# Kernel tuning notes

Hardware: AMD Instinct MI355X
Metric: run time of the kernel (lower is better)

## Reference

```python
import jax, jax.numpy as jnp
import numpy as np

N, E, D, R = 8192, 131072, 128, 32
SIZES = (3, 5, 7)  # per-degree component counts (2l+1)
LN_EPS = 1e-5


def setup_inputs() -> dict:
    key = jax.random.key(0)
    ks = jax.random.split(key, 20)
    rn = lambda k, shape, s=1.0: jax.random.normal(k, shape, jnp.float32) * s
    inp = {
        'X0': rn(ks[0], (N, SIZES[0], D)),
        'X1': rn(ks[1], (N, SIZES[1], D)),
        'X2': rn(ks[2], (N, SIZES[2], D)),
        't_ij': rn(ks[3], (E, D)),
        'r0': rn(ks[4], (E, SIZES[0])),
        'r1': rn(ks[5], (E, SIZES[1])),
        'r2': rn(ks[6], (E, SIZES[2])),
        'edge_index': jax.random.randint(ks[7], (2, E), 0, N, dtype=jnp.int32),
        # params
        'W_vq': rn(ks[8], (D, R), D ** -0.5),
        'W_vk0': rn(ks[9], (D, R), D ** -0.5),
        'W_vk1': rn(ks[10], (D, R), D ** -0.5),
        'W_vk2': rn(ks[11], (D, R), D ** -0.5),
        'ln_g': jnp.ones((R,), jnp.float32),
        'ln_b': jnp.zeros((R,), jnp.float32),
        'W_w': rn(ks[12], (R, D), R ** -0.5),
        'b_w': jnp.zeros((D,), jnp.float32),
        'W_t1': rn(ks[13], (D, D), D ** -0.5),
        'b_t1': jnp.zeros((D,), jnp.float32),
        'W_t2': rn(ks[14], (D, D), D ** -0.5),
        'b_t2': jnp.zeros((D,), jnp.float32),
    }
    return inp


def _vec_rej(x, r):
    # x: [E, L, R], r: [E, L]; dot over component dim (L), keepdim, subtract projection
    r = r[..., None]
    dot = jnp.sum(x * r, axis=1, keepdims=True)  # [E, 1, R]
    return x - dot * r


def reference(X0, X1, X2, t_ij, r0, r1, r2, edge_index,
              W_vq, W_vk0, W_vk1, W_vk2, ln_g, ln_b, W_w, b_w,
              W_t1, b_t1, W_t2, b_t2):
    n_j, n_i = edge_index[0], edge_index[1]
    X_ls = jnp.concatenate([X0, X1, X2], axis=1)                 # [N, 15, D]
    eq_i = jnp.einsum('nld,dr->nlr', X_ls, W_vq)[n_i]            # [E, 15, R]
    ek = jnp.concatenate([
        jnp.einsum('nld,dr->nlr', X0, W_vk0),
        jnp.einsum('nld,dr->nlr', X1, W_vk1),
        jnp.einsum('nld,dr->nlr', X2, W_vk2)], axis=1)
    ek_j = ek[n_j]                                               # [E, 15, R]
    # per-degree vector rejection (vec_rej=True)
    qs, ksl, off = [], [], 0
    for r in (r0, r1, r2):
        s = r.shape[1]
        qs.append(_vec_rej(eq_i[:, off:off + s], r))
        ksl.append(_vec_rej(ek_j[:, off:off + s], -r))
        off += s
    eq_i = jnp.concatenate(qs, axis=1)
    ek_j = jnp.concatenate(ksl, axis=1)
    w_ij = jnp.sum(eq_i * ek_j, axis=1)                          # [E, R]
    # mlp_w = LayerNorm + Linear
    mu = jnp.mean(w_ij, axis=-1, keepdims=True)
    var = jnp.var(w_ij, axis=-1, keepdims=True)
    wn = (w_ij - mu) * jax.lax.rsqrt(var + LN_EPS) * ln_g + ln_b
    dw = wn @ W_w + b_w                                          # [E, D]
    # mlp_t = Linear -> silu -> Linear, then outer activation
    t = jax.nn.silu(t_ij @ W_t1 + b_t1) @ W_t2 + b_t2            # [E, D]
    return dw * jax.nn.silu(t)
```

## Files before the change

kernel.cpp:

```cpp
#include <hip/hip_runtime.h>
#include <hip/hip_bf16.h>

#define N_NODES 8192
#define N_EDGES 131072
#define LN_EPS  1e-5f

typedef __attribute__((ext_vector_type(8))) short bf16x8;
typedef __attribute__((ext_vector_type(4))) short bf16x4;
typedef __attribute__((ext_vector_type(4))) float f32x4;

__device__ __forceinline__ float silu_f(float x) {
    return x * __builtin_amdgcn_rcpf(1.0f + __expf(-x));
}

__device__ __forceinline__ unsigned short f2bf(float x) {
    union { float f; unsigned int u; } v; v.f = x;
    unsigned int r = v.u + 0x7FFFu + ((v.u >> 16) & 1u);
    return (unsigned short)(r >> 16);
}
__device__ __forceinline__ float bf2f(unsigned short u) {
    union { float f; unsigned int x; } v; v.x = ((unsigned int)u) << 16;
    return v.f;
}
__device__ __forceinline__ unsigned int pk2(float a, float b) {
    float2 t; t.x = a; t.y = b;
    union { __hip_bfloat162 h; unsigned int u; } v;
    v.h = __float22bfloat162_rn(t);
    return v.u;
}
__device__ __forceinline__ bf16x8 pack8(float4 u, float4 v) {
    union { bf16x8 b; unsigned int w[4]; } o;
    o.w[0] = pk2(u.x, u.y); o.w[1] = pk2(u.z, u.w);
    o.w[2] = pk2(v.x, v.y); o.w[3] = pk2(v.z, v.w);
    return o.b;
}
__device__ __forceinline__ bf16x4 pack4(float a, float b, float c, float d) {
    union { bf16x4 v; unsigned int u[2]; } o;
    o.u[0] = pk2(a, b); o.u[1] = pk2(c, d);
    return o.v;
}
__device__ __forceinline__ f32x4 mfma16(bf16x8 a, bf16x8 b, f32x4 c) {
    return __builtin_amdgcn_mfma_f32_16x16x32_bf16(a, b, c, 0, 0, 0);
}
#if __has_builtin(__builtin_amdgcn_mfma_f32_16x16x16bf16_1k)
__device__ __forceinline__ f32x4 mfma_k16(bf16x4 a, bf16x4 b, f32x4 c) {
    return __builtin_amdgcn_mfma_f32_16x16x16bf16_1k(a, b, c, 0, 0, 0);
}
#else
__device__ __forceinline__ f32x4 mfma_k16(bf16x4 a, bf16x4 b, f32x4 c) {
    f32x4 d;
    asm("v_mfma_f32_16x16x16_bf16 %0, %1, %2, %3"
        : "=v"(d) : "v"(a), "v"(b), "v"(c));
    return d;
}
#endif

__global__ __launch_bounds__(256) void prep_kernel(
    const float* __restrict__ W_w, const float* __restrict__ W_t1,
    const float* __restrict__ W_t2, const float* __restrict__ Wvq,
    const float* __restrict__ Wvk0, const float* __restrict__ Wvk1,
    const float* __restrict__ Wvk2,
    unsigned short* __restrict__ Wtw, unsigned short* __restrict__ Wt1b,
    unsigned short* __restrict__ Wt2b, unsigned short* __restrict__ Wqt,
    unsigned short* __restrict__ Wk0t, unsigned short* __restrict__ Wk1t,
    unsigned short* __restrict__ Wk2t)
{
    int i = blockIdx.x * 256 + threadIdx.x;
    if (i < 16384) {
        int n = i >> 7, k = i & 127;
        Wt1b[i] = f2bf(W_t1[k * 128 + n]);
        Wt2b[i] = f2bf(W_t2[k * 128 + n]);
    }
    if (i < 4096) {
        { int n = i >> 5, k = i & 31; Wtw[i] = f2bf(W_w[k * 128 + n]); }
        int r = i >> 7, d = i & 127;
        Wqt[i]  = f2bf(Wvq [d * 32 + r]);
        Wk0t[i] = f2bf(Wvk0[d * 32 + r]);
        Wk1t[i] = f2bf(Wvk1[d * 32 + r]);
        Wk2t[i] = f2bf(Wvk2[d * 32 + r]);
    }
}

template<int S, int LOFF>
__device__ __forceinline__ void proj_body(
    const float* __restrict__ X, const unsigned short* __restrict__ Wqt,
    const unsigned short* __restrict__ Wkt,
    unsigned short* __restrict__ eq, unsigned short* __restrict__ ek,
    int row0)
{
    const int tid  = threadIdx.x;
    const int lane = tid & 63;
    const int wv   = tid >> 6;
    const int l15  = lane & 15;
    const int lk   = lane >> 4;
    const int xrow = row0 + wv * 16 + l15;

    bf16x8 xf[4];
    #pragma unroll
    for (int kt = 0; kt < 4; ++kt) {
        const float* p = X + (size_t)xrow * 128 + kt * 32 + lk * 8;
        xf[kt] = pack8(*(const float4*)p, *(const float4*)(p + 4));
    }

    f32x4 qa[2], ka[2];
    #pragma unroll
    for (int h = 0; h < 2; ++h) {
        qa[h] = (f32x4){0.f, 0.f, 0.f, 0.f};
        ka[h] = (f32x4){0.f, 0.f, 0.f, 0.f};
    }
    #pragma unroll
    for (int kt = 0; kt < 4; ++kt) {
        #pragma unroll
        for (int h = 0; h < 2; ++h) {
            bf16x8 wq = *(const bf16x8*)&Wqt[(h * 16 + l15) * 128 + kt * 32 + lk * 8];
            bf16x8 wk = *(const bf16x8*)&Wkt[(h * 16 + l15) * 128 + kt * 32 + lk * 8];
            qa[h] = mfma16(wq, xf[kt], qa[h]);
            ka[h] = mfma16(wk, xf[kt], ka[h]);
        }
    }

    const int n = xrow / S;
    const int l = xrow % S + LOFF;
    const size_t base = (size_t)n * 512 + (size_t)l * 32;
    #pragma unroll
    for (int h = 0; h < 2; ++h) {
        union { ushort4 s; unsigned int u[2]; } pq, pk_;
        pq.u[0]  = pk2(qa[h][0], qa[h][1]); pq.u[1]  = pk2(qa[h][2], qa[h][3]);
        pk_.u[0] = pk2(ka[h][0], ka[h][1]); pk_.u[1] = pk2(ka[h][2], ka[h][3]);
        *(ushort4*)&eq[base + h * 16 + lk * 4] = pq.s;
        *(ushort4*)&ek[base + h * 16 + lk * 4] = pk_.s;
    }
}

__global__ __launch_bounds__(256) void proj_kernel(
    const float* __restrict__ X0, const float* __restrict__ X1,
    const float* __restrict__ X2,
    const unsigned short* __restrict__ Wqt,
    const unsigned short* __restrict__ Wk0t,
    const unsigned short* __restrict__ Wk1t,
    const unsigned short* __restrict__ Wk2t,
    unsigned short* __restrict__ eq, unsigned short* __restrict__ ek)
{
    const int b = blockIdx.x;
    if (b < 384)
        proj_body<3, 0>(X0, Wqt, Wk0t, eq, ek, b * 64);
    else if (b < 1024)
        proj_body<5, 3>(X1, Wqt, Wk1t, eq, ek, (b - 384) * 64);
    else
        proj_body<7, 8>(X2, Wqt, Wk2t, eq, ek, (b - 1024) * 64);
}

__device__ __forceinline__ float edge_w_f(
    const float* qv, const float* kv, const float* rv)
{
    float qk = 0.f;
    #pragma unroll
    for (int l = 0; l < 15; ++l) qk = fmaf(qv[l], kv[l], qk);
    float c0 = 2.f, c1 = 2.f, c2 = 2.f;
    #pragma unroll
    for (int l = 0; l < 3; ++l)  c0 -= rv[l] * rv[l];
    #pragma unroll
    for (int l = 3; l < 8; ++l)  c1 -= rv[l] * rv[l];
    #pragma unroll
    for (int l = 8; l < 15; ++l) c2 -= rv[l] * rv[l];
    float dq0 = 0.f, dk0 = 0.f, dq1 = 0.f, dk1 = 0.f, dq2 = 0.f, dk2 = 0.f;
    #pragma unroll
    for (int l = 0; l < 3; ++l)  { dq0 = fmaf(qv[l], rv[l], dq0); dk0 = fmaf(kv[l], rv[l], dk0); }
    #pragma unroll
    for (int l = 3; l < 8; ++l)  { dq1 = fmaf(qv[l], rv[l], dq1); dk1 = fmaf(kv[l], rv[l], dk1); }
    #pragma unroll
    for (int l = 8; l < 15; ++l) { dq2 = fmaf(qv[l], rv[l], dq2); dk2 = fmaf(kv[l], rv[l], dk2); }
    return qk - dq0 * dk0 * c0 - dq1 * dk1 * c1 - dq2 * dk2 * c2;
}

__global__ __launch_bounds__(256) void wn_kernel(
    const unsigned short* __restrict__ eq, const unsigned short* __restrict__ ek,
    const float* __restrict__ r0, const float* __restrict__ r1,
    const float* __restrict__ r2, const int* __restrict__ eidx,
    const float* __restrict__ ln_g, const float* __restrict__ ln_b,
    unsigned short* __restrict__ wn)
{
    const int tid = threadIdx.x;
    const int r   = tid & 31;
    const int hw  = tid >> 5;
    const int e0  = blockIdx.x * 16 + hw * 2;
    const int e1  = e0 + 1;
    const float g  = ln_g[r];
    const float bb = ln_b[r];

    const int nj0 = eidx[e0], ni0 = eidx[N_EDGES + e0];
    const int nj1 = eidx[e1], ni1 = eidx[N_EDGES + e1];

    const unsigned short* qp0 = eq + (size_t)ni0 * 512 + r;
    const unsigned short* kp0 = ek + (size_t)nj0 * 512 + r;
    const unsigned short* qp1 = eq + (size_t)ni1 * 512 + r;
    const unsigned short* kp1 = ek + (size_t)nj1 * 512 + r;

    float qv0[15], kv0[15], qv1[15], kv1[15];
    #pragma unroll
    for (int l = 0; l < 15; ++l) {
        qv0[l] = bf2f(qp0[l * 32]);
        kv0[l] = bf2f(kp0[l * 32]);
        qv1[l] = bf2f(qp1[l * 32]);
        kv1[l] = bf2f(kp1[l * 32]);
    }

    float rva[15], rvb[15];
    #pragma unroll
    for (int c = 0; c < 3; ++c) { rva[c]     = r0[e0 * 3 + c]; rvb[c]     = r0[e1 * 3 + c]; }
    #pragma unroll
    for (int c = 0; c < 5; ++c) { rva[3 + c] = r1[e0 * 5 + c]; rvb[3 + c] = r1[e1 * 5 + c]; }
    #pragma unroll
    for (int c = 0; c < 7; ++c) { rva[8 + c] = r2[e0 * 7 + c]; rvb[8 + c] = r2[e1 * 7 + c]; }

    const float w0 = edge_w_f(qv0, kv0, rva);
    const float w1 = edge_w_f(qv1, kv1, rvb);

    float s0 = w0, s20 = w0 * w0, s1 = w1, s21 = w1 * w1;
    #pragma unroll
    for (int off = 1; off < 32; off <<= 1) {
        s0  += __shfl_xor(s0,  off); s20 += __shfl_xor(s20, off);
        s1  += __shfl_xor(s1,  off); s21 += __shfl_xor(s21, off);
    }
    const float mu0   = s0 * (1.f / 32.f);
    const float var0  = s20 * (1.f / 32.f) - mu0 * mu0;
    const float mu1   = s1 * (1.f / 32.f);
    const float var1  = s21 * (1.f / 32.f) - mu1 * mu1;
    wn[(size_t)e0 * 32 + r] = f2bf((w0 - mu0) * rsqrtf(var0 + LN_EPS) * g + bb);
    wn[(size_t)e1 * 32 + r] = f2bf((w1 - mu1) * rsqrtf(var1 + LN_EPS) * g + bb);
}

__global__ __launch_bounds__(512, 4) void edge_kernel(
    const float* __restrict__ t_ij,
    const unsigned short* __restrict__ wn,
    const unsigned short* __restrict__ Wtw, const float* __restrict__ b_w,
    const unsigned short* __restrict__ Wt1, const float* __restrict__ b_t1,
    const unsigned short* __restrict__ Wt2, const float* __restrict__ b_t2,
    float* __restrict__ out)
{
    __shared__ __align__(16) unsigned short W1l[16384];
    __shared__ __align__(16) unsigned short W2l[16384];
    __shared__ __align__(16) unsigned short Wwl[4096];

    const int tid  = threadIdx.x;
    const int lane = tid & 63;
    const int wv   = tid >> 6;
    const int l15  = lane & 15;
    const int lk   = lane >> 4;
    const int tile = (blockIdx.x * 8 + wv) * 32;
    const int swz7 = (l15 & 7) << 4;
    const int swz3 = (l15 & 3) << 4;

    #pragma unroll
    for (int i = 0; i < 4; ++i) {
        const int c   = tid + i * 512;
        const int row = c >> 4, c16 = c & 15;
        const int off = (row * 256 + c16 * 16) ^ ((row & 7) << 4);
        *(uint4*)((char*)W1l + off) = *(const uint4*)&Wt1[row * 128 + c16 * 8];
        *(uint4*)((char*)W2l + off) = *(const uint4*)&Wt2[row * 128 + c16 * 8];
    }
    {
        const int c   = tid;
        const int row = c >> 2, c4 = c & 3;
        uint4 v = *(const uint4*)&Wtw[row * 32 + c4 * 8];
        *(uint4*)((char*)Wwl + ((row * 64 + c4 * 16) ^ ((row & 3) << 4))) = v;
    }

    bf16x8 a1[4][2];
    #pragma unroll
    for (int kt = 0; kt < 4; ++kt)
        #pragma unroll
        for (int rt = 0; rt < 2; ++rt) {
            const float* p = t_ij + (size_t)(tile + rt * 16 + l15) * 128
                           + kt * 32 + lk * 8;
            a1[kt][rt] = pack8(*(const float4*)p, *(const float4*)(p + 4));
        }

    bf16x8 wnf[2];
    #pragma unroll
    for (int rt = 0; rt < 2; ++rt)
        wnf[rt] = *(const bf16x8*)&wn[(size_t)(tile + rt * 16 + l15) * 32 + lk * 8];

    __syncthreads();

    bf16x4 h[2][8];
    #pragma unroll
    for (int ct = 0; ct < 8; ++ct) {
        bf16x8 w1f[4];
        #pragma unroll
        for (int kt = 0; kt < 4; ++kt)
            w1f[kt] = *(const bf16x8*)((const char*)W1l +
                (((ct * 16 + l15) * 256 + kt * 64 + lk * 16) ^ swz7));
        f32x4 ac[2];
        #pragma unroll
        for (int rt = 0; rt < 2; ++rt) ac[rt] = (f32x4){0.f, 0.f, 0.f, 0.f};
        #pragma unroll
        for (int kt = 0; kt < 4; ++kt)
            #pragma unroll
            for (int rt = 0; rt < 2; ++rt)
                ac[rt] = mfma16(w1f[kt], a1[kt][rt], ac[rt]);

        const float4 bt1 = *(const float4*)&b_t1[ct * 16 + lk * 4];
        #pragma unroll
        for (int rt = 0; rt < 2; ++rt)
            h[rt][ct] = pack4(silu_f(ac[rt][0] + bt1.x),
                              silu_f(ac[rt][1] + bt1.y),
                              silu_f(ac[rt][2] + bt1.z),
                              silu_f(ac[rt][3] + bt1.w));
    }

    #pragma unroll
    for (int ct2 = 0; ct2 < 8; ++ct2) {
        bf16x4 w2b[8];
        #pragma unroll
        for (int ct1 = 0; ct1 < 8; ++ct1)
            w2b[ct1] = *(const bf16x4*)((const char*)W2l +
                (((ct2 * 16 + l15) * 256 + ct1 * 32 + lk * 8) ^ swz7));
        bf16x8 wwf = *(const bf16x8*)((const char*)Wwl +
            (((ct2 * 16 + l15) * 64 + lk * 16) ^ swz3));
        const float bwv = b_w[ct2 * 16 + l15];
        const float b2v = b_t2[ct2 * 16 + l15];

        #pragma unroll
        for (int rt = 0; rt < 2; ++rt) {
            f32x4 o = (f32x4){0.f, 0.f, 0.f, 0.f};
            #pragma unroll
            for (int ct1 = 0; ct1 < 8; ++ct1)
                o = mfma_k16(h[rt][ct1], w2b[ct1], o);
            f32x4 d = mfma16(wnf[rt], wwf, (f32x4){0.f, 0.f, 0.f, 0.f});

            float* op = out + (size_t)(tile + rt * 16 + lk * 4) * 128
                      + ct2 * 16 + l15;
            #pragma unroll
            for (int j = 0; j < 4; ++j)
                op[j * 128] = (d[j] + bwv) * silu_f(o[j] + b2v);
        }
    }
}

extern "C" void kernel_launch(void* const* d_in, const int* in_sizes, int n_in,
                              void* d_out, int out_size, void* d_ws, size_t ws_size,
                              hipStream_t stream) {
    (void)in_sizes; (void)n_in; (void)out_size; (void)ws_size;
    const float* X0   = (const float*)d_in[0];
    const float* X1   = (const float*)d_in[1];
    const float* X2   = (const float*)d_in[2];
    const float* t_ij = (const float*)d_in[3];
    const float* r0   = (const float*)d_in[4];
    const float* r1   = (const float*)d_in[5];
    const float* r2   = (const float*)d_in[6];
    const int*   eidx = (const int*)d_in[7];
    const float* Wvq  = (const float*)d_in[8];
    const float* Wvk0 = (const float*)d_in[9];
    const float* Wvk1 = (const float*)d_in[10];
    const float* Wvk2 = (const float*)d_in[11];
    const float* ln_g = (const float*)d_in[12];
    const float* ln_b = (const float*)d_in[13];
    const float* W_w  = (const float*)d_in[14];
    const float* b_w  = (const float*)d_in[15];
    const float* W_t1 = (const float*)d_in[16];
    const float* b_t1 = (const float*)d_in[17];
    const float* W_t2 = (const float*)d_in[18];
    const float* b_t2 = (const float*)d_in[19];
    float* out = (float*)d_out;

    unsigned short* eq   = (unsigned short*)d_ws;
    unsigned short* ek   = eq  + (size_t)N_NODES * 512;
    unsigned short* wn   = ek  + (size_t)N_NODES * 512;
    unsigned short* Wtw  = wn  + (size_t)N_EDGES * 32;
    unsigned short* Wt1b = Wtw  + 4096;
    unsigned short* Wt2b = Wt1b + 16384;
    unsigned short* Wqt  = Wt2b + 16384;
    unsigned short* Wk0t = Wqt  + 4096;
    unsigned short* Wk1t = Wk0t + 4096;
    unsigned short* Wk2t = Wk1t + 4096;

    prep_kernel<<<64, 256, 0, stream>>>(W_w, W_t1, W_t2, Wvq, Wvk0, Wvk1, Wvk2,
                                        Wtw, Wt1b, Wt2b, Wqt, Wk0t, Wk1t, Wk2t);
    proj_kernel<<<1920, 256, 0, stream>>>(X0, X1, X2, Wqt, Wk0t, Wk1t, Wk2t,
                                          eq, ek);
    wn_kernel<<<N_EDGES / 16, 256, 0, stream>>>(eq, ek, r0, r1, r2, eidx,
                                                ln_g, ln_b, wn);
    edge_kernel<<<N_EDGES / 256, 512, 0, stream>>>(t_ij, wn, Wtw, b_w,
                                                   Wt1b, b_t1, Wt2b, b_t2, out);
}
```

Baseline: 94.50 us.

## Pre-swizzle weights in global and load to LDS via direct global_load_lds

The prep kernel now writes the MLP and W_w weights already in the XOR-swizzled layout the edge kernel uses in LDS. The edge kernel can then fill shared memory with direct global-to-LDS loads instead of staging the data through registers. MFMA sections are also wrapped in s_setprio to raise wave priority during the matrix math. This cuts register pressure and VALU/LDS-store instructions in the prologue, but it relies on global_load_lds semantics and on the swizzle mapping being correct.

```diff
diff --git a/kernel.cpp b/kernel.cpp
--- a/kernel.cpp
+++ b/kernel.cpp
@@ -55,24 +55,32 @@
 }
 #endif
 
+__device__ __forceinline__ void gload_lds16(const void* g, void* l) {
+    __builtin_amdgcn_global_load_lds(
+        (const __attribute__((address_space(1))) unsigned int*)g,
+        (__attribute__((address_space(3))) unsigned int*)l, 16, 0, 0);
+}
+
 __global__ __launch_bounds__(256) void prep_kernel(
     const float* __restrict__ W_w, const float* __restrict__ W_t1,
     const float* __restrict__ W_t2, const float* __restrict__ Wvq,
     const float* __restrict__ Wvk0, const float* __restrict__ Wvk1,
     const float* __restrict__ Wvk2,
-    unsigned short* __restrict__ Wtw, unsigned short* __restrict__ Wt1b,
-    unsigned short* __restrict__ Wt2b, unsigned short* __restrict__ Wqt,
+    unsigned short* __restrict__ W1s, unsigned short* __restrict__ W2s,
+    unsigned short* __restrict__ Wws, unsigned short* __restrict__ Wqt,
     unsigned short* __restrict__ Wk0t, unsigned short* __restrict__ Wk1t,
     unsigned short* __restrict__ Wk2t)
 {
     int i = blockIdx.x * 256 + threadIdx.x;
     if (i < 16384) {
-        int n = i >> 7, k = i & 127;
-        Wt1b[i] = f2bf(W_t1[k * 128 + n]);
-        Wt2b[i] = f2bf(W_t2[k * 128 + n]);
+        int n  = i >> 7;
+        int kk = (i & 127) ^ ((n & 7) << 3);
+        W1s[i] = f2bf(W_t1[kk * 128 + n]);
+        W2s[i] = f2bf(W_t2[kk * 128 + n]);
     }
     if (i < 4096) {
-        { int n = i >> 5, k = i & 31; Wtw[i] = f2bf(W_w[k * 128 + n]); }
+        { int n = i >> 5; int r = (i & 31) ^ ((n & 3) << 3);
+          Wws[i] = f2bf(W_w[r * 128 + n]); }
         int r = i >> 7, d = i & 127;
         Wqt[i]  = f2bf(Wvq [d * 32 + r]);
         Wk0t[i] = f2bf(Wvk0[d * 32 + r]);
@@ -233,9 +241,9 @@
 __global__ __launch_bounds__(512, 4) void edge_kernel(
     const float* __restrict__ t_ij,
     const unsigned short* __restrict__ wn,
-    const unsigned short* __restrict__ Wtw, const float* __restrict__ b_w,
-    const unsigned short* __restrict__ Wt1, const float* __restrict__ b_t1,
-    const unsigned short* __restrict__ Wt2, const float* __restrict__ b_t2,
+    const unsigned short* __restrict__ Wws, const float* __restrict__ b_w,
+    const unsigned short* __restrict__ W1s, const float* __restrict__ b_t1,
+    const unsigned short* __restrict__ W2s, const float* __restrict__ b_t2,
     float* __restrict__ out)
 {
     __shared__ __align__(16) unsigned short W1l[16384];
@@ -251,19 +259,17 @@
     const int swz7 = (l15 & 7) << 4;
     const int swz3 = (l15 & 3) << 4;
 
-    #pragma unroll
-    for (int i = 0; i < 4; ++i) {
-        const int c   = tid + i * 512;
-        const int row = c >> 4, c16 = c & 15;
-        const int off = (row * 256 + c16 * 16) ^ ((row & 7) << 4);
-        *(uint4*)((char*)W1l + off) = *(const uint4*)&Wt1[row * 128 + c16 * 8];
-        *(uint4*)((char*)W2l + off) = *(const uint4*)&Wt2[row * 128 + c16 * 8];
-    }
     {
-        const int c   = tid;
-        const int row = c >> 2, c4 = c & 3;
-        uint4 v = *(const uint4*)&Wtw[row * 32 + c4 * 8];
-        *(uint4*)((char*)Wwl + ((row * 64 + c4 * 16) ^ ((row & 3) << 4))) = v;
+        const char* s1 = (const char*)W1s;
+        const char* s2 = (const char*)W2s;
+        #pragma unroll
+        for (int i = 0; i < 4; ++i) {
+            const int boff = wv * 4096 + i * 1024;
+            gload_lds16(s1 + boff + lane * 16, (char*)W1l + boff);
+            gload_lds16(s2 + boff + lane * 16, (char*)W2l + boff);
+        }
+        const int boffw = wv * 1024;
+        gload_lds16((const char*)Wws + boffw + lane * 16, (char*)Wwl + boffw);
     }
 
     bf16x8 a1[4][2];
@@ -294,11 +300,13 @@
         f32x4 ac[2];
         #pragma unroll
         for (int rt = 0; rt < 2; ++rt) ac[rt] = (f32x4){0.f, 0.f, 0.f, 0.f};
+        __builtin_amdgcn_s_setprio(1);
         #pragma unroll
         for (int kt = 0; kt < 4; ++kt)
             #pragma unroll
             for (int rt = 0; rt < 2; ++rt)
                 ac[rt] = mfma16(w1f[kt], a1[kt][rt], ac[rt]);
+        __builtin_amdgcn_s_setprio(0);
 
         const float4 bt1 = *(const float4*)&b_t1[ct * 16 + lk * 4];
         #pragma unroll
@@ -324,10 +332,12 @@
         #pragma unroll
         for (int rt = 0; rt < 2; ++rt) {
             f32x4 o = (f32x4){0.f, 0.f, 0.f, 0.f};
+            __builtin_amdgcn_s_setprio(1);
             #pragma unroll
             for (int ct1 = 0; ct1 < 8; ++ct1)
                 o = mfma_k16(h[rt][ct1], w2b[ct1], o);
             f32x4 d = mfma16(wnf[rt], wwf, (f32x4){0.f, 0.f, 0.f, 0.f});
+            __builtin_amdgcn_s_setprio(0);
 
             float* op = out + (size_t)(tile + rt * 16 + lk * 4) * 128
                       + ct2 * 16 + l15;
@@ -367,20 +377,20 @@
     unsigned short* eq   = (unsigned short*)d_ws;
     unsigned short* ek   = eq  + (size_t)N_NODES * 512;
     unsigned short* wn   = ek  + (size_t)N_NODES * 512;
-    unsigned short* Wtw  = wn  + (size_t)N_EDGES * 32;
-    unsigned short* Wt1b = Wtw  + 4096;
-    unsigned short* Wt2b = Wt1b + 16384;
-    unsigned short* Wqt  = Wt2b + 16384;
+    unsigned short* Wqt  = wn  + (size_t)N_EDGES * 32;
     unsigned short* Wk0t = Wqt  + 4096;
     unsigned short* Wk1t = Wk0t + 4096;
     unsigned short* Wk2t = Wk1t + 4096;
+    unsigned short* W1s  = Wk2t + 4096;
+    unsigned short* W2s  = W1s  + 16384;
+    unsigned short* Wws  = W2s  + 16384;
 
     prep_kernel<<<64, 256, 0, stream>>>(W_w, W_t1, W_t2, Wvq, Wvk0, Wvk1, Wvk2,
-                                        Wtw, Wt1b, Wt2b, Wqt, Wk0t, Wk1t, Wk2t);
+                                        W1s, W2s, Wws, Wqt, Wk0t, Wk1t, Wk2t);
     proj_kernel<<<1920, 256, 0, stream>>>(X0, X1, X2, Wqt, Wk0t, Wk1t, Wk2t,
                                           eq, ek);
     wn_kernel<<<N_EDGES / 16, 256, 0, stream>>>(eq, ek, r0, r1, r2, eidx,
                                                 ln_g, ln_b, wn);
-    edge_kernel<<<N_EDGES / 256, 512, 0, stream>>>(t_ij, wn, Wtw, b_w,
-                                                   Wt1b, b_t1, Wt2b, b_t2, out);
-}
+    edge_kernel<<<N_EDGES / 256, 512, 0, stream>>>(t_ij, wn, Wws, b_w,
+                                                   W1s, b_t1, W2s, b_t2, out);
+}
```

Result: slower. 96.80 us (+2.4%).

## Halve edge tile per wave and reuse one LDS buffer for W_t1 then W_t2

Applied to the files above, without the earlier changes.

Each wave in edge_kernel now handles 16 edges instead of 32, which roughly halves its register state. The W_t2 weights are loaded into the same LDS buffer as W_t1 after the first GEMM finishes, so per-block LDS drops from about 72KB to 40KB. Launch bounds move to 8 blocks and the grid doubles, all aimed at higher occupancy to hide memory latency. In exchange, every block reloads both weight matrices for half as many edges, which doubles weight-staging traffic, and two extra barriers sit between the GEMMs.

```diff
diff --git a/kernel.cpp b/kernel.cpp
--- a/kernel.cpp
+++ b/kernel.cpp
@@ -230,7 +230,7 @@
     wn[(size_t)e1 * 32 + r] = f2bf((w1 - mu1) * rsqrtf(var1 + LN_EPS) * g + bb);
 }
 
-__global__ __launch_bounds__(512, 4) void edge_kernel(
+__global__ __launch_bounds__(512, 8) void edge_kernel(
     const float* __restrict__ t_ij,
     const unsigned short* __restrict__ wn,
     const unsigned short* __restrict__ Wtw, const float* __restrict__ b_w,
@@ -239,7 +239,6 @@
     float* __restrict__ out)
 {
     __shared__ __align__(16) unsigned short W1l[16384];
-    __shared__ __align__(16) unsigned short W2l[16384];
     __shared__ __align__(16) unsigned short Wwl[4096];
 
     const int tid  = threadIdx.x;
@@ -247,7 +246,7 @@
     const int wv   = tid >> 6;
     const int l15  = lane & 15;
     const int lk   = lane >> 4;
-    const int tile = (blockIdx.x * 8 + wv) * 32;
+    const int tile = (blockIdx.x * 8 + wv) * 16;
     const int swz7 = (l15 & 7) << 4;
     const int swz3 = (l15 & 3) << 4;
 
@@ -257,7 +256,6 @@
         const int row = c >> 4, c16 = c & 15;
         const int off = (row * 256 + c16 * 16) ^ ((row & 7) << 4);
         *(uint4*)((char*)W1l + off) = *(const uint4*)&Wt1[row * 128 + c16 * 8];
-        *(uint4*)((char*)W2l + off) = *(const uint4*)&Wt2[row * 128 + c16 * 8];
     }
     {
         const int c   = tid;
@@ -266,24 +264,18 @@
         *(uint4*)((char*)Wwl + ((row * 64 + c4 * 16) ^ ((row & 3) << 4))) = v;
     }
 
-    bf16x8 a1[4][2];
-    #pragma unroll
-    for (int kt = 0; kt < 4; ++kt)
-        #pragma unroll
-        for (int rt = 0; rt < 2; ++rt) {
-            const float* p = t_ij + (size_t)(tile + rt * 16 + l15) * 128
-                           + kt * 32 + lk * 8;
-            a1[kt][rt] = pack8(*(const float4*)p, *(const float4*)(p + 4));
-        }
-
-    bf16x8 wnf[2];
-    #pragma unroll
-    for (int rt = 0; rt < 2; ++rt)
-        wnf[rt] = *(const bf16x8*)&wn[(size_t)(tile + rt * 16 + l15) * 32 + lk * 8];
+    bf16x8 a1[4];
+    #pragma unroll
+    for (int kt = 0; kt < 4; ++kt) {
+        const float* p = t_ij + (size_t)(tile + l15) * 128 + kt * 32 + lk * 8;
+        a1[kt] = pack8(*(const float4*)p, *(const float4*)(p + 4));
+    }
+
+    bf16x8 wnf = *(const bf16x8*)&wn[(size_t)(tile + l15) * 32 + lk * 8];
 
     __syncthreads();
 
-    bf16x4 h[2][8];
+    bf16x4 h[8];
     #pragma unroll
     for (int ct = 0; ct < 8; ++ct) {
         bf16x8 w1f[4];
@@ -291,50 +283,49 @@
         for (int kt = 0; kt < 4; ++kt)
             w1f[kt] = *(const bf16x8*)((const char*)W1l +
                 (((ct * 16 + l15) * 256 + kt * 64 + lk * 16) ^ swz7));
-        f32x4 ac[2];
-        #pragma unroll
-        for (int rt = 0; rt < 2; ++rt) ac[rt] = (f32x4){0.f, 0.f, 0.f, 0.f};
+        f32x4 ac = (f32x4){0.f, 0.f, 0.f, 0.f};
         #pragma unroll
         for (int kt = 0; kt < 4; ++kt)
-            #pragma unroll
-            for (int rt = 0; rt < 2; ++rt)
-                ac[rt] = mfma16(w1f[kt], a1[kt][rt], ac[rt]);
+            ac = mfma16(w1f[kt], a1[kt], ac);
 
         const float4 bt1 = *(const float4*)&b_t1[ct * 16 + lk * 4];
-        #pragma unroll
-        for (int rt = 0; rt < 2; ++rt)
-            h[rt][ct] = pack4(silu_f(ac[rt][0] + bt1.x),
-                              silu_f(ac[rt][1] + bt1.y),
-                              silu_f(ac[rt][2] + bt1.z),
-                              silu_f(ac[rt][3] + bt1.w));
-    }
+        h[ct] = pack4(silu_f(ac[0] + bt1.x), silu_f(ac[1] + bt1.y),
+                      silu_f(ac[2] + bt1.z), silu_f(ac[3] + bt1.w));
+    }
+
+    __syncthreads();
+
+    #pragma unroll
+    for (int i = 0; i < 4; ++i) {
+        const int c   = tid + i * 512;
+        const int row = c >> 4, c16 = c & 15;
+        const int off = (row * 256 + c16 * 16) ^ ((row & 7) << 4);
+        *(uint4*)((char*)W1l + off) = *(const uint4*)&Wt2[row * 128 + c16 * 8];
+    }
+    __syncthreads();
 
     #pragma unroll
     for (int ct2 = 0; ct2 < 8; ++ct2) {
         bf16x4 w2b[8];
         #pragma unroll
         for (int ct1 = 0; ct1 < 8; ++ct1)
-            w2b[ct1] = *(const bf16x4*)((const char*)W2l +
+            w2b[ct1] = *(const bf16x4*)((const char*)W1l +
                 (((ct2 * 16 + l15) * 256 + ct1 * 32 + lk * 8) ^ swz7));
         bf16x8 wwf = *(const bf16x8*)((const char*)Wwl +
             (((ct2 * 16 + l15) * 64 + lk * 16) ^ swz3));
         const float bwv = b_w[ct2 * 16 + l15];
         const float b2v = b_t2[ct2 * 16 + l15];
 
-        #pragma unroll
-        for (int rt = 0; rt < 2; ++rt) {
-            f32x4 o = (f32x4){0.f, 0.f, 0.f, 0.f};
-            #pragma unroll
-            for (int ct1 = 0; ct1 < 8; ++ct1)
-                o = mfma_k16(h[rt][ct1], w2b[ct1], o);
-            f32x4 d = mfma16(wnf[rt], wwf, (f32x4){0.f, 0.f, 0.f, 0.f});
-
-            float* op = out + (size_t)(tile + rt * 16 + lk * 4) * 128
-                      + ct2 * 16 + l15;
-            #pragma unroll
-            for (int j = 0; j < 4; ++j)
-                op[j * 128] = (d[j] + bwv) * silu_f(o[j] + b2v);
-        }
+        f32x4 o = (f32x4){0.f, 0.f, 0.f, 0.f};
+        #pragma unroll
+        for (int ct1 = 0; ct1 < 8; ++ct1)
+            o = mfma_k16(h[ct1], w2b[ct1], o);
+        f32x4 d = mfma16(wnf, wwf, (f32x4){0.f, 0.f, 0.f, 0.f});
+
+        float* op = out + (size_t)(tile + lk * 4) * 128 + ct2 * 16 + l15;
+        #pragma unroll
+        for (int j = 0; j < 4; ++j)
+            op[j * 128] = (d[j] + bwv) * silu_f(o[j] + b2v);
     }
 }
 
@@ -381,6 +372,6 @@
                                           eq, ek);
     wn_kernel<<<N_EDGES / 16, 256, 0, stream>>>(eq, ek, r0, r1, r2, eidx,
                                                 ln_g, ln_b, wn);
-    edge_kernel<<<N_EDGES / 256, 512, 0, stream>>>(t_ij, wn, Wtw, b_w,
+    edge_kernel<<<N_EDGES / 128, 512, 0, stream>>>(t_ij, wn, Wtw, b_w,
                                                    Wt1b, b_t1, Wt2b, b_t2, out);
 }
```

Result: slower. 100.3 us (+6.1%).
